# Performance work log

Measured on AMD Instinct MI355X. Metric: run time of the kernel, lower is better.

Reference implementation:

```python
import jax, jax.numpy as jnp
import numpy as np

DMODEL = 1024
HEADS = 16
KEY_DIM = DMODEL // HEADS


def setup_inputs() -> dict:
    key = jax.random.key(0)
    k0, k1, k2, k3, k4 = jax.random.split(key, 5)
    scale = 1.0 / np.sqrt(DMODEL)
    return {
        "inputs": jax.random.normal(k0, (2, 2048, DMODEL), dtype=jnp.float32),
        "Wq": jax.random.normal(k1, (DMODEL, DMODEL), dtype=jnp.float32) * scale,
        "Wk": jax.random.normal(k2, (DMODEL, DMODEL), dtype=jnp.float32) * scale,
        "Wv": jax.random.normal(k3, (DMODEL, DMODEL), dtype=jnp.float32) * scale,
        "Wo": jax.random.normal(k4, (DMODEL, DMODEL), dtype=jnp.float32) * scale,
    }


def reference(inputs, Wq, Wk, Wv, Wo):
    B, S, _ = inputs.shape
    # nn.Linear(bias=False): y = x @ W.T ; then reshape to (B, S, H, Dh) and transpose to (B, H, S, Dh)
    def proj(W):
        return (inputs @ W.T).reshape(B, S, HEADS, KEY_DIM).transpose(0, 2, 1, 3)

    q, k, v = proj(Wq), proj(Wk), proj(Wv)
    scale = 1.0 / np.sqrt(KEY_DIM).astype(np.float32)
    score = jnp.einsum('bhsd,bhtd->bhst', q, k) * scale  # [B,H,S,S]
    attn = jax.nn.softmax(score, axis=-1)
    out = jnp.einsum('bhst,bhtd->bhsd', attn, v)  # [B,H,S,Dh]
    out = out.transpose(0, 2, 1, 3).reshape(B, S, HEADS * KEY_DIM)
    return out @ Wo.T
```

## Files before the change

kernel.cpp:

```cpp
#include <hip/hip_runtime.h>
#include <hip/hip_bf16.h>
#include <stdint.h>

typedef __attribute__((ext_vector_type(8))) short short8;
typedef __attribute__((ext_vector_type(4))) float floatx4;

#define MFMA16(a, b, c) __builtin_amdgcn_mfma_f32_16x16x32_bf16((a), (b), (c), 0, 0, 0)

static __device__ __forceinline__ uint16_t f2bf(float f) {
  union { float f; uint32_t u; } x; x.f = f;
  uint32_t r = x.u + 0x7fffu + ((x.u >> 16) & 1u);
  return (uint16_t)(r >> 16);
}

static __device__ __forceinline__ uint32_t cvtpk_bf16(float lo, float hi) {
  uint32_t r;
  asm("v_cvt_pk_bf16_f32 %0, %1, %2" : "=v"(r) : "v"(lo), "v"(hi));
  return r;
}

constexpr int DM = 1024, NH = 16, KD = 64, NB = 2, SQ = 2048;
constexpr int MTOT = NB * SQ;
constexpr int NT = SQ / 64;
constexpr int NP = NT / 2;

__global__ void convert_kernel(const float* __restrict__ X,
                               const float* __restrict__ Wq, const float* __restrict__ Wk,
                               const float* __restrict__ Wv, const float* __restrict__ Wo,
                               uint16_t* __restrict__ Xb, uint16_t* __restrict__ Wqkvb,
                               uint16_t* __restrict__ Wob) {
  const int NX = MTOT * DM;
  const int NW = DM * DM;
  const int TOT8 = (NX + 4 * NW) / 8;
  for (int t = blockIdx.x * blockDim.x + threadIdx.x; t < TOT8; t += gridDim.x * blockDim.x) {
    int i = t * 8;
    const float* src; uint16_t* dst;
    if (i < NX) { src = X + i; dst = Xb + i; }
    else if (i < NX + 3 * NW) {
      int j = i - NX; dst = Wqkvb + j;
      src = (j < NW) ? (Wq + j) : (j < 2 * NW) ? (Wk + (j - NW)) : (Wv + (j - 2 * NW));
    } else {
      int j = i - NX - 3 * NW; src = Wo + j; dst = Wob + j;
    }
    float4 a = ((const float4*)src)[0];
    float4 b = ((const float4*)src)[1];
    ushort4 o0, o1;
    o0.x = f2bf(a.x); o0.y = f2bf(a.y); o0.z = f2bf(a.z); o0.w = f2bf(a.w);
    o1.x = f2bf(b.x); o1.y = f2bf(b.y); o1.z = f2bf(b.z); o1.w = f2bf(b.w);
    ((ushort4*)dst)[0] = o0;
    ((ushort4*)dst)[1] = o1;
  }
}

__global__ __launch_bounds__(256) void gemm_qkv(const uint16_t* __restrict__ Aq,
                                                const uint16_t* __restrict__ Bq,
                                                uint16_t* __restrict__ Qb, uint16_t* __restrict__ Kb,
                                                uint16_t* __restrict__ VTb) {
  __shared__ uint16_t Al[128 * 32];
  __shared__ uint16_t Bl[128 * 32];
  const int K = 1024;
  const int Ntiles = 24;
  int nwg = gridDim.x;
  int bid = (blockIdx.x & 7) * (nwg >> 3) + (blockIdx.x >> 3);
  int bm = bid / Ntiles, bn = bid % Ntiles;
  int brow = bm * 128, bcol = bn * 128;
  int tid = threadIdx.x;
  int w = tid >> 6, lane = tid & 63, g = lane >> 4, c16 = lane & 15;
  int wm = w >> 1, wn = w & 1;
  int rr = tid >> 2;
  int ce = (tid & 3) * 8;

  floatx4 acc[4][4] = {};

  for (int k0 = 0; k0 < K; k0 += 32) {
    __syncthreads();
#pragma unroll
    for (int c = 0; c < 2; ++c) {
      __builtin_amdgcn_global_load_lds(
          (const __attribute__((address_space(1))) void*)(Aq + (size_t)(brow + c * 64 + rr) * K + k0 + ce),
          (__attribute__((address_space(3))) void*)((char*)Al + c * 4096 + w * 1024), 16, 0, 0);
      __builtin_amdgcn_global_load_lds(
          (const __attribute__((address_space(1))) void*)(Bq + (size_t)(bcol + c * 64 + rr) * K + k0 + ce),
          (__attribute__((address_space(3))) void*)((char*)Bl + c * 4096 + w * 1024), 16, 0, 0);
    }
    __syncthreads();
    short8 af[4], bf[4];
#pragma unroll
    for (int mt = 0; mt < 4; ++mt)
      af[mt] = *(const short8*)&Al[(wm * 64 + mt * 16 + c16) * 32 + g * 8];
#pragma unroll
    for (int nt = 0; nt < 4; ++nt)
      bf[nt] = *(const short8*)&Bl[(wn * 64 + nt * 16 + c16) * 32 + g * 8];
#pragma unroll
    for (int mt = 0; mt < 4; ++mt)
#pragma unroll
      for (int nt = 0; nt < 4; ++nt)
        acc[mt][nt] = MFMA16(af[mt], bf[nt], acc[mt][nt]);
  }

#pragma unroll
  for (int mt = 0; mt < 4; ++mt) {
#pragma unroll
    for (int nt = 0; nt < 4; ++nt) {
      int n = bcol + wn * 64 + nt * 16 + c16;
#pragma unroll
      for (int r = 0; r < 4; ++r) {
        int m = brow + wm * 64 + mt * 16 + g * 4 + r;
        float v = acc[mt][nt][r];
        int proj = n >> 10;
        int hd = n & 1023;
        int h = hd >> 6, d = hd & 63;
        int b = m >> 11, s = m & 2047;
        size_t bh = (size_t)(b * NH + h);
        if (proj == 0) {
          Qb[(bh * SQ + s) * KD + d] = f2bf(v * 0.18033688011112042f);
        } else if (proj == 1) {
          int st = s >> 4, r2 = s & 15, k8 = d >> 3, j = d & 7;
          Kb[bh * (size_t)(SQ * KD) + (((size_t)(st * 8 + k8) * 16 + r2) * 8 + j)] = f2bf(v);
        } else {
          int kt = s >> 6, kvl = s & 63;
          int c = kvl >> 5, tth = (kvl >> 4) & 1, gg = (kvl >> 2) & 3, rs = kvl & 3;
          int jp = tth * 4 + rs;
          int dt = d >> 4, cc = d & 15;
          VTb[bh * (size_t)(SQ * KD) + (size_t)kt * 4096 +
              (size_t)((c * 4 + dt) * 512 + gg * 128 + cc * 8 + jp)] = f2bf(v);
        }
      }
    }
  }
}

__global__ __launch_bounds__(256) void gemm_out64(const uint16_t* __restrict__ Aq,
                                                  const uint16_t* __restrict__ Bq,
                                                  float* __restrict__ Out) {
  __shared__ uint16_t Al[64 * 32];
  __shared__ uint16_t Bl[128 * 32];
  const int K = 1024;
  int nwg = gridDim.x;
  int bid = (blockIdx.x & 7) * (nwg >> 3) + (blockIdx.x >> 3);
  int bm = bid >> 3, bn = bid & 7;
  int brow = bm * 64, bcol = bn * 128;
  int tid = threadIdx.x;
  int w = tid >> 6, lane = tid & 63, g = lane >> 4, c16 = lane & 15;
  int wm = w >> 1, wn = w & 1;
  int rr = tid >> 2;
  int ce = (tid & 3) * 8;

  floatx4 acc[2][4] = {};

  for (int k0 = 0; k0 < K; k0 += 32) {
    __syncthreads();
    __builtin_amdgcn_global_load_lds(
        (const __attribute__((address_space(1))) void*)(Aq + (size_t)(brow + rr) * K + k0 + ce),
        (__attribute__((address_space(3))) void*)((char*)Al + w * 1024), 16, 0, 0);
#pragma unroll
    for (int c = 0; c < 2; ++c) {
      __builtin_amdgcn_global_load_lds(
          (const __attribute__((address_space(1))) void*)(Bq + (size_t)(bcol + c * 64 + rr) * K + k0 + ce),
          (__attribute__((address_space(3))) void*)((char*)Bl + c * 4096 + w * 1024), 16, 0, 0);
    }
    __syncthreads();
    short8 af[2], bf[4];
#pragma unroll
    for (int mt = 0; mt < 2; ++mt)
      af[mt] = *(const short8*)&Al[(wm * 32 + mt * 16 + c16) * 32 + g * 8];
#pragma unroll
    for (int nt = 0; nt < 4; ++nt)
      bf[nt] = *(const short8*)&Bl[(wn * 64 + nt * 16 + c16) * 32 + g * 8];
#pragma unroll
    for (int mt = 0; mt < 2; ++mt)
#pragma unroll
      for (int nt = 0; nt < 4; ++nt)
        acc[mt][nt] = MFMA16(af[mt], bf[nt], acc[mt][nt]);
  }

#pragma unroll
  for (int mt = 0; mt < 2; ++mt) {
#pragma unroll
    for (int nt = 0; nt < 4; ++nt) {
      int n = bcol + wn * 64 + nt * 16 + c16;
#pragma unroll
      for (int r = 0; r < 4; ++r) {
        int m = brow + wm * 32 + mt * 16 + g * 4 + r;
        Out[(size_t)m * DM + n] = acc[mt][nt][r];
      }
    }
  }
}

__global__ __launch_bounds__(512, 4) void attn_kernel(const uint16_t* __restrict__ Q,
                                                      const uint16_t* __restrict__ Kt,
                                                      const uint16_t* __restrict__ Vt,
                                                      uint16_t* __restrict__ O) {
  __shared__ __attribute__((aligned(16))) uint16_t Kbuf[2][8192];
  __shared__ __attribute__((aligned(16))) uint16_t Vbuf[2][8192];

  int bid = blockIdx.x;
  int bh = bid & 31, qt = bid >> 5;
  int qb = qt * 128;
  int b = bh >> 4, h = bh & 15;
  int tid = threadIdx.x, lane = tid & 63, wv = tid >> 6, g = lane >> 4, c16 = lane & 15;

  const uint16_t* Qh = Q + (size_t)bh * SQ * KD;
  const uint16_t* Kh = Kt + (size_t)bh * SQ * KD;
  const uint16_t* Vh = Vt + (size_t)bh * SQ * KD;

  int qrow = qb + wv * 16 + c16;
  short8 qf0 = *(const short8*)&Qh[(size_t)qrow * KD + g * 8];
  short8 qf1 = *(const short8*)&Qh[(size_t)qrow * KD + 32 + g * 8];

  float l = 0.0f;
  floatx4 accO[4] = {};
  const floatx4 SHIFT_INIT = {-16.0f, -16.0f, -16.0f, -16.0f};

  auto stage = [&](int buf, int pair) {
    size_t base = (size_t)pair * 8192;
#pragma unroll
    for (int i = 0; i < 2; ++i) {
      __builtin_amdgcn_global_load_lds(
          (const __attribute__((address_space(1))) void*)(Kh + base + wv * 1024 + i * 512 + lane * 8),
          (__attribute__((address_space(3))) void*)((char*)&Kbuf[buf][0] + wv * 2048 + i * 1024), 16, 0, 0);
      __builtin_amdgcn_global_load_lds(
          (const __attribute__((address_space(1))) void*)(Vh + base + wv * 1024 + i * 512 + lane * 8),
          (__attribute__((address_space(3))) void*)((char*)&Vbuf[buf][0] + wv * 2048 + i * 1024), 16, 0, 0);
    }
  };

  stage(0, 0);
  __syncthreads();

  for (int p = 0; p < NP; ++p) {
    int cur = p & 1;
    int pn = (p + 1 < NP) ? (p + 1) : p;
    stage(cur ^ 1, pn);

#pragma unroll
    for (int sub = 0; sub < 2; ++sub) {
      const char* kb = (const char*)&Kbuf[cur][sub * 4096];
      const char* vb = (const char*)&Vbuf[cur][sub * 4096];
      short8 kf[4][2], vf[2][4];
#pragma unroll
      for (int tt = 0; tt < 4; ++tt)
#pragma unroll
        for (int hf = 0; hf < 2; ++hf)
          kf[tt][hf] = *(const short8*)(kb + tt * 2048 + hf * 1024 + lane * 16);
#pragma unroll
      for (int c = 0; c < 2; ++c)
#pragma unroll
        for (int dt = 0; dt < 4; ++dt)
          vf[c][dt] = *(const short8*)(vb + (c * 4 + dt) * 1024 + lane * 16);

      floatx4 sacc[4];
#pragma unroll
      for (int tt = 0; tt < 4; ++tt) sacc[tt] = SHIFT_INIT;
      __builtin_amdgcn_s_setprio(1);
#pragma unroll
      for (int tt = 0; tt < 4; ++tt) {
        sacc[tt] = MFMA16(kf[tt][0], qf0, sacc[tt]);
        sacc[tt] = MFMA16(kf[tt][1], qf1, sacc[tt]);
      }
      __builtin_amdgcn_s_setprio(0);

#pragma unroll
      for (int tt = 0; tt < 4; ++tt)
#pragma unroll
        for (int r = 0; r < 4; ++r)
          sacc[tt][r] = exp2f(sacc[tt][r]);
      float s01 = (sacc[0][0] + sacc[0][1]) + (sacc[0][2] + sacc[0][3]);
      float s23 = (sacc[1][0] + sacc[1][1]) + (sacc[1][2] + sacc[1][3]);
      float s45 = (sacc[2][0] + sacc[2][1]) + (sacc[2][2] + sacc[2][3]);
      float s67 = (sacc[3][0] + sacc[3][1]) + (sacc[3][2] + sacc[3][3]);
      l += (s01 + s23) + (s45 + s67);

      union { uint32_t u[4]; short8 s8; } pa[2];
#pragma unroll
      for (int c = 0; c < 2; ++c) {
        pa[c].u[0] = cvtpk_bf16(sacc[2 * c][0], sacc[2 * c][1]);
        pa[c].u[1] = cvtpk_bf16(sacc[2 * c][2], sacc[2 * c][3]);
        pa[c].u[2] = cvtpk_bf16(sacc[2 * c + 1][0], sacc[2 * c + 1][1]);
        pa[c].u[3] = cvtpk_bf16(sacc[2 * c + 1][2], sacc[2 * c + 1][3]);
      }
      __builtin_amdgcn_s_setprio(1);
#pragma unroll
      for (int c = 0; c < 2; ++c)
#pragma unroll
        for (int dt = 0; dt < 4; ++dt)
          accO[dt] = MFMA16(pa[c].s8, vf[c][dt], accO[dt]);
      __builtin_amdgcn_s_setprio(0);
    }

    __syncthreads();
  }

  l += __shfl_xor(l, 16);
  l += __shfl_xor(l, 32);

  float lv[4];
#pragma unroll
  for (int r = 0; r < 4; ++r) lv[r] = 1.0f / __shfl(l, g * 4 + r);
#pragma unroll
  for (int dt = 0; dt < 4; ++dt) {
#pragma unroll
    for (int r = 0; r < 4; ++r) {
      int s = qb + wv * 16 + g * 4 + r;
      int d = dt * 16 + c16;
      O[((size_t)(b * SQ + s)) * DM + h * KD + d] = f2bf(accO[dt][r] * lv[r]);
    }
  }
}

extern "C" void kernel_launch(void* const* d_in, const int* in_sizes, int n_in,
                              void* d_out, int out_size, void* d_ws, size_t ws_size,
                              hipStream_t stream) {
  const float* X = (const float*)d_in[0];
  const float* Wq = (const float*)d_in[1];
  const float* Wk = (const float*)d_in[2];
  const float* Wv = (const float*)d_in[3];
  const float* Wo = (const float*)d_in[4];
  float* out = (float*)d_out;

  char* ws = (char*)d_ws;
  uint16_t* Xb    = (uint16_t*)(ws);
  uint16_t* Wqkvb = (uint16_t*)(ws + 8388608);
  uint16_t* Wob   = (uint16_t*)(ws + 14680064);
  uint16_t* Qb    = (uint16_t*)(ws + 16777216);
  uint16_t* Kb    = (uint16_t*)(ws + 25165824);
  uint16_t* VTb   = (uint16_t*)(ws + 33554432);
  uint16_t* Ob    = (uint16_t*)(ws + 41943040);

  hipLaunchKernelGGL(convert_kernel, dim3(1024), dim3(256), 0, stream,
                     X, Wq, Wk, Wv, Wo, Xb, Wqkvb, Wob);
  hipLaunchKernelGGL(gemm_qkv, dim3(32 * 24), dim3(256), 0, stream,
                     Xb, Wqkvb, Qb, Kb, VTb);
  hipLaunchKernelGGL(attn_kernel, dim3(512), dim3(512), 0, stream,
                     Qb, Kb, VTb, Ob);
  hipLaunchKernelGGL(gemm_out64, dim3(512), dim3(256), 0, stream,
                     Ob, Wob, out);
}
```

Baseline: 195.1 us.

## Double GEMM K-tile to 64 and XOR-swizzle LDS layout in projection GEMMs

Both the QKV projection GEMM and the output projection GEMM now stage 64-wide K slices instead of 32, which halves the number of barrier pairs per K loop and doubles the MFMA work per sync. The global-to-LDS loads are written with an XOR swizzle on 16-byte chunks keyed by row, and the fragment reads apply the matching swizzle to avoid LDS bank conflicts at the 128-byte row stride. LDS use per block doubles, which could lower occupancy, and the attention kernel is unchanged.

Result: slower. 199.6 us (+2.3%).

```diff
diff --git a/kernel.cpp b/kernel.cpp
--- a/kernel.cpp
+++ b/kernel.cpp
@@ -56,8 +56,8 @@
                                                 const uint16_t* __restrict__ Bq,
                                                 uint16_t* __restrict__ Qb, uint16_t* __restrict__ Kb,
                                                 uint16_t* __restrict__ VTb) {
-  __shared__ uint16_t Al[128 * 32];
-  __shared__ uint16_t Bl[128 * 32];
+  __shared__ uint16_t Al[128 * 64];
+  __shared__ uint16_t Bl[128 * 64];
   const int K = 1024;
   const int Ntiles = 24;
   int nwg = gridDim.x;
@@ -67,35 +67,40 @@
   int tid = threadIdx.x;
   int w = tid >> 6, lane = tid & 63, g = lane >> 4, c16 = lane & 15;
   int wm = w >> 1, wn = w & 1;
-  int rr = tid >> 2;
-  int ce = (tid & 3) * 8;
+  int rr = tid >> 3;
+  int ces = ((tid & 7) ^ (rr & 7)) * 8;
 
   floatx4 acc[4][4] = {};
 
-  for (int k0 = 0; k0 < K; k0 += 32) {
-    __syncthreads();
-#pragma unroll
-    for (int c = 0; c < 2; ++c) {
-      __builtin_amdgcn_global_load_lds(
-          (const __attribute__((address_space(1))) void*)(Aq + (size_t)(brow + c * 64 + rr) * K + k0 + ce),
-          (__attribute__((address_space(3))) void*)((char*)Al + c * 4096 + w * 1024), 16, 0, 0);
-      __builtin_amdgcn_global_load_lds(
-          (const __attribute__((address_space(1))) void*)(Bq + (size_t)(bcol + c * 64 + rr) * K + k0 + ce),
-          (__attribute__((address_space(3))) void*)((char*)Bl + c * 4096 + w * 1024), 16, 0, 0);
-    }
-    __syncthreads();
-    short8 af[4], bf[4];
-#pragma unroll
-    for (int mt = 0; mt < 4; ++mt)
-      af[mt] = *(const short8*)&Al[(wm * 64 + mt * 16 + c16) * 32 + g * 8];
-#pragma unroll
-    for (int nt = 0; nt < 4; ++nt)
-      bf[nt] = *(const short8*)&Bl[(wn * 64 + nt * 16 + c16) * 32 + g * 8];
-#pragma unroll
-    for (int mt = 0; mt < 4; ++mt)
+  for (int k0 = 0; k0 < K; k0 += 64) {
+    __syncthreads();
+#pragma unroll
+    for (int i = 0; i < 4; ++i) {
+      __builtin_amdgcn_global_load_lds(
+          (const __attribute__((address_space(1))) void*)(Aq + (size_t)(brow + i * 32 + rr) * K + k0 + ces),
+          (__attribute__((address_space(3))) void*)((char*)Al + i * 4096 + w * 1024), 16, 0, 0);
+      __builtin_amdgcn_global_load_lds(
+          (const __attribute__((address_space(1))) void*)(Bq + (size_t)(bcol + i * 32 + rr) * K + k0 + ces),
+          (__attribute__((address_space(3))) void*)((char*)Bl + i * 4096 + w * 1024), 16, 0, 0);
+    }
+    __syncthreads();
+#pragma unroll
+    for (int kk = 0; kk < 2; ++kk) {
+      short8 af[4], bf[4];
+#pragma unroll
+      for (int mt = 0; mt < 4; ++mt)
+        af[mt] = *(const short8*)((const char*)Al + (wm * 64 + mt * 16 + c16) * 128 +
+                                  (((kk * 4 + g) ^ (c16 & 7)) << 4));
 #pragma unroll
       for (int nt = 0; nt < 4; ++nt)
-        acc[mt][nt] = MFMA16(af[mt], bf[nt], acc[mt][nt]);
+        bf[nt] = *(const short8*)((const char*)Bl + (wn * 64 + nt * 16 + c16) * 128 +
+                                  (((kk * 4 + g) ^ (c16 & 7)) << 4));
+#pragma unroll
+      for (int mt = 0; mt < 4; ++mt)
+#pragma unroll
+        for (int nt = 0; nt < 4; ++nt)
+          acc[mt][nt] = MFMA16(af[mt], bf[nt], acc[mt][nt]);
+    }
   }
 
 #pragma unroll
@@ -133,8 +138,8 @@
 __global__ __launch_bounds__(256) void gemm_out64(const uint16_t* __restrict__ Aq,
                                                   const uint16_t* __restrict__ Bq,
                                                   float* __restrict__ Out) {
-  __shared__ uint16_t Al[64 * 32];
-  __shared__ uint16_t Bl[128 * 32];
+  __shared__ uint16_t Al[64 * 64];
+  __shared__ uint16_t Bl[128 * 64];
   const int K = 1024;
   int nwg = gridDim.x;
   int bid = (blockIdx.x & 7) * (nwg >> 3) + (blockIdx.x >> 3);
@@ -143,35 +148,41 @@
   int tid = threadIdx.x;
   int w = tid >> 6, lane = tid & 63, g = lane >> 4, c16 = lane & 15;
   int wm = w >> 1, wn = w & 1;
-  int rr = tid >> 2;
-  int ce = (tid & 3) * 8;
+  int rr = tid >> 3;
+  int ces = ((tid & 7) ^ (rr & 7)) * 8;
 
   floatx4 acc[2][4] = {};
 
-  for (int k0 = 0; k0 < K; k0 += 32) {
-    __syncthreads();
-    __builtin_amdgcn_global_load_lds(
-        (const __attribute__((address_space(1))) void*)(Aq + (size_t)(brow + rr) * K + k0 + ce),
-        (__attribute__((address_space(3))) void*)((char*)Al + w * 1024), 16, 0, 0);
-#pragma unroll
-    for (int c = 0; c < 2; ++c) {
-      __builtin_amdgcn_global_load_lds(
-          (const __attribute__((address_space(1))) void*)(Bq + (size_t)(bcol + c * 64 + rr) * K + k0 + ce),
-          (__attribute__((address_space(3))) void*)((char*)Bl + c * 4096 + w * 1024), 16, 0, 0);
-    }
-    __syncthreads();
-    short8 af[2], bf[4];
-#pragma unroll
-    for (int mt = 0; mt < 2; ++mt)
-      af[mt] = *(const short8*)&Al[(wm * 32 + mt * 16 + c16) * 32 + g * 8];
-#pragma unroll
-    for (int nt = 0; nt < 4; ++nt)
-      bf[nt] = *(const short8*)&Bl[(wn * 64 + nt * 16 + c16) * 32 + g * 8];
-#pragma unroll
-    for (int mt = 0; mt < 2; ++mt)
+  for (int k0 = 0; k0 < K; k0 += 64) {
+    __syncthreads();
+#pragma unroll
+    for (int i = 0; i < 2; ++i)
+      __builtin_amdgcn_global_load_lds(
+          (const __attribute__((address_space(1))) void*)(Aq + (size_t)(brow + i * 32 + rr) * K + k0 + ces),
+          (__attribute__((address_space(3))) void*)((char*)Al + i * 4096 + w * 1024), 16, 0, 0);
+#pragma unroll
+    for (int i = 0; i < 4; ++i)
+      __builtin_amdgcn_global_load_lds(
+          (const __attribute__((address_space(1))) void*)(Bq + (size_t)(bcol + i * 32 + rr) * K + k0 + ces),
+          (__attribute__((address_space(3))) void*)((char*)Bl + i * 4096 + w * 1024), 16, 0, 0);
+    __syncthreads();
+#pragma unroll
+    for (int kk = 0; kk < 2; ++kk) {
+      short8 af[2], bf[4];
+#pragma unroll
+      for (int mt = 0; mt < 2; ++mt)
+        af[mt] = *(const short8*)((const char*)Al + (wm * 32 + mt * 16 + c16) * 128 +
+                                  (((kk * 4 + g) ^ (c16 & 7)) << 4));
 #pragma unroll
       for (int nt = 0; nt < 4; ++nt)
-        acc[mt][nt] = MFMA16(af[mt], bf[nt], acc[mt][nt]);
+        bf[nt] = *(const short8*)((const char*)Bl + (wn * 64 + nt * 16 + c16) * 128 +
+                                  (((kk * 4 + g) ^ (c16 & 7)) << 4));
+#pragma unroll
+      for (int mt = 0; mt < 2; ++mt)
+#pragma unroll
+        for (int nt = 0; nt < 4; ++nt)
+          acc[mt][nt] = MFMA16(af[mt], bf[nt], acc[mt][nt]);
+    }
   }
 
 #pragma unroll
```
